# Optimization experiments

Hardware: AMD Instinct MI355X
Metric: run time of the kernel (lower is better)

The kernel has to match this reference:

```python
import jax, jax.numpy as jnp
import numpy as np

NUM_USERS = 100000
USER_EMB_DIM = 64
PROC_DIM = 128          # Dense(128) embedding_processor
NUM_SHARDS = 16
MEM_SIZE = 512          # memory slots per shard
WORD_SIZE = 64
NUM_READS = 4
INPUT_SIZE = 256
B, S = 256, 128
IN_DIM = INPUT_SIZE + PROC_DIM  # combined controller input width


def setup_inputs() -> dict:
    key = jax.random.key(0)
    k = jax.random.split(key, 7)
    x = jax.random.normal(k[0], (B, S, INPUT_SIZE), dtype=jnp.float32)
    user_id = jax.random.randint(k[1], (B,), 0, NUM_USERS, dtype=jnp.int64)
    user_emb_table = jax.random.normal(k[2], (NUM_USERS, USER_EMB_DIM), dtype=jnp.float32) * 0.02
    W_proc = jax.random.normal(k[3], (USER_EMB_DIM, PROC_DIM), dtype=jnp.float32) * (1.0 / np.sqrt(USER_EMB_DIM))
    b_proc = jnp.zeros((PROC_DIM,), dtype=jnp.float32)
    # per-shard parameters: query projection + memory matrix (the shard's state)
    Wq = jax.random.normal(k[4], (NUM_SHARDS, IN_DIM, NUM_READS * WORD_SIZE), dtype=jnp.float32) * (1.0 / np.sqrt(IN_DIM))
    memory = jax.random.normal(k[5], (NUM_SHARDS, MEM_SIZE, WORD_SIZE), dtype=jnp.float32)
    return {"x": x, "user_id": user_id, "user_emb_table": user_emb_table,
            "W_proc": W_proc, "b_proc": b_proc, "Wq": Wq, "memory": memory}


def reference(x, user_id, user_emb_table, W_proc, b_proc, Wq, memory):
    # user embedding lookup + Dense processor
    ue = user_emb_table[user_id]                       # [B, E]
    pe = ue @ W_proc + b_proc                          # [B, PROC_DIM]
    # broadcast the processed embedding across the sequence and concat on features
    pe_seq = jnp.broadcast_to(pe[:, None, :], (x.shape[0], x.shape[1], pe.shape[-1]))
    combined = jnp.concatenate([x, pe_seq], axis=-1)   # [B, S, IN_DIM]
    # shard routing (irregular gather of per-shard params)
    sid = user_id % NUM_SHARDS                         # [B]
    Wq_g = Wq[sid]                                     # [B, IN_DIM, R*W]
    mem_g = memory[sid]                                # [B, M, W]
    # per-sample shard forward: content-based read
    q = jnp.einsum('bsi,bio->bso', combined, Wq_g)     # [B, S, R*W]
    q = q.reshape(q.shape[0], q.shape[1], NUM_READS, WORD_SIZE)
    scores = jnp.einsum('bsrw,bmw->bsrm', q, mem_g)    # [B, S, R, M]
    wts = jax.nn.softmax(scores, axis=-1)
    read_words = jnp.einsum('bsrm,bmw->bsrw', wts, mem_g)  # [B, S, R, W]
    # original code keeps final_states[-1] (last sample's state)
    final_state = wts[-1]                              # [S, R, M]
    return read_words, final_state
```

## Files before the change

### kernel.cpp

```cpp
#include <hip/hip_runtime.h>
#include <math.h>

#define BB 256
#define SSEQ 128
#define INPUT 256
#define PD 128
#define EE 64
#define RW 256
#define MM 512
#define WW 64
#define KD 384

typedef _Float16 half8 __attribute__((ext_vector_type(8)));
typedef __fp16 fp16x2 __attribute__((ext_vector_type(2)));
typedef float float4v __attribute__((ext_vector_type(4)));

#define LOG2E 1.44269504088896f
#define OUT1 8388608u

#define MEMT_OFF 65536
#define F32_OFF  131072
#define LDS_BYTES (131072 + 3840)
#define UE_O 0
#define PE_O 64
#define QPE_O 192
#define QP_O 448

union H8 { half8 h8; unsigned int u[4]; uint4 u4; };

__device__ __forceinline__ unsigned int pk2(float a, float b) {
    union { fp16x2 h; unsigned int u; } p;
    p.h = __builtin_amdgcn_cvt_pkrtz(a, b);
    return p.u;
}

__global__ void wqt_kernel(const float* __restrict__ Wq, _Float16* __restrict__ WqT) {
    __shared__ float tile[64][65];
    const int kt = blockIdx.x, nt = blockIdx.y, sid = blockIdx.z;
    const float* src = Wq + (size_t)sid*KD*RW + (size_t)(kt*64)*RW + nt*64;
    for (int i = 0; i < 16; ++i) {
        int idx = i*256 + threadIdx.x;
        int kk = idx >> 6, nn = idx & 63;
        tile[kk][nn] = src[(size_t)kk*RW + nn];
    }
    __syncthreads();
    _Float16* dst = WqT + (size_t)sid*RW*KD + (size_t)(nt*64)*KD + kt*64;
    for (int i = 0; i < 16; ++i) {
        int idx = i*256 + threadIdx.x;
        int nn = idx >> 6, kk = idx & 63;
        dst[(size_t)nn*KD + kk] = (_Float16)tile[kk][nn];
    }
}

__global__ void __launch_bounds__(512, 2)
attn_kernel(const float* __restrict__ x, const int* __restrict__ user_id,
            const float* __restrict__ uet, const float* __restrict__ W_proc,
            const float* __restrict__ b_proc, const float* __restrict__ Wq,
            const float* __restrict__ memG, const _Float16* __restrict__ WqT,
            int useWqT, float* __restrict__ out)
{
    extern __shared__ char smraw[];
    unsigned short* smemu = (unsigned short*)smraw;
    uint4* sm128 = (uint4*)smraw;
    float* smf = (float*)(smraw + F32_OFF);

    const int t = threadIdx.x;
    const int b = blockIdx.x;
    const int halfb = blockIdx.y;
    const int lane = t & 63, wv = t >> 6;
    const int n16 = lane & 15, quad = lane >> 4;
    const int r = wv & 3, sq = wv >> 2;
    const int s0 = halfb*64 + sq*32;
    const int swz = n16 & 7;

    const int uid = user_id[b];
    const int sid = uid & 15;
    const float* memB = memG + (size_t)sid * (MM*WW);

    if (t < EE) smf[UE_O + t] = uet[(size_t)uid*EE + t];

    for (int i = 0; i < 8; ++i) {
        int id = t + i*512;
        int m = id >> 3, cw = id & 7;
        const float* g = memB + m*64 + cw*8;
        float4 a0 = *(const float4*)g;
        float4 a1 = *(const float4*)(g + 4);
        int c2 = cw ^ (m & 7);
        sm128[(m*128 + (c2<<4)) >> 4] =
            make_uint4(pk2(a0.x,a0.y), pk2(a0.z,a0.w), pk2(a1.x,a1.y), pk2(a1.z,a1.w));
    }
    __syncthreads();

    for (int i = 0; i < 8; ++i) {
        int id = t + i*512;
        int w = id & 63, cm = id >> 6;
        unsigned int uu[4];
        #pragma unroll
        for (int p = 0; p < 4; ++p) {
            int m0 = cm*8 + 2*p, m1 = m0 + 1;
            unsigned short lo = smemu[m0*64 + (((w>>3) ^ (m0&7))<<3) + (w&7)];
            unsigned short hi = smemu[m1*64 + (((w>>3) ^ (m1&7))<<3) + (w&7)];
            uu[p] = (unsigned int)lo | ((unsigned int)hi << 16);
        }
        sm128[(MEMT_OFF + w*1024 + ((cm ^ (w&7))<<4)) >> 4] = make_uint4(uu[0],uu[1],uu[2],uu[3]);
    }
    if (t < PD) {
        float a = b_proc[t];
        #pragma unroll
        for (int e = 0; e < EE; ++e) a = fmaf(smf[UE_O + e], W_proc[e*PD + t], a);
        smf[PE_O + t] = a;
    }
    __syncthreads();
    {
        int n = t & 255, h = t >> 8;
        float s = 0.f;
        const float* wr = Wq + (size_t)sid*KD*RW + (size_t)(256 + h*64)*RW + n;
        #pragma unroll 8
        for (int k = 0; k < 64; ++k) s = fmaf(smf[PE_O + h*64 + k], wr[(size_t)k*RW], s);
        smf[QP_O + h*256 + n] = s;
    }
    __syncthreads();
    if (t < 256) smf[QPE_O + t] = LOG2E * (smf[QP_O + t] + smf[QP_O + 256 + t]);
    __syncthreads();


    float4v qacc[4][2];
    #pragma unroll
    for (int mt = 0; mt < 4; ++mt)
        #pragma unroll
        for (int nt = 0; nt < 2; ++nt) qacc[mt][nt] = (float4v)0.f;

    const float* xB = x + (size_t)(b*SSEQ + s0) * INPUT;
    for (int kc = 0; kc < 8; ++kc) {
        H8 afr[4];
        if (useWqT) {
            const _Float16* wt0 = WqT + (size_t)sid*RW*KD + (size_t)(r*64)*KD + kc*32 + quad*8;
            #pragma unroll
            for (int mt = 0; mt < 4; ++mt)
                afr[mt].u4 = *(const uint4*)(wt0 + (size_t)(mt*16 + n16)*KD);
        } else {
            const float* wq0 = Wq + (size_t)sid*KD*RW + (size_t)(kc*32 + quad*8)*RW + r*64 + n16;
            #pragma unroll
            for (int mt = 0; mt < 4; ++mt)
                #pragma unroll
                for (int p = 0; p < 4; ++p)
                    afr[mt].u[p] = pk2(wq0[(size_t)(2*p)*RW + mt*16],
                                       wq0[(size_t)(2*p+1)*RW + mt*16]);
        }
        H8 bfr[2];
        #pragma unroll
        for (int nt = 0; nt < 2; ++nt) {
            const float* xg = xB + (size_t)(nt*16 + n16)*INPUT + kc*32 + quad*8;
            float4 a0 = *(const float4*)xg;
            float4 a1 = *(const float4*)(xg + 4);
            bfr[nt].u[0] = pk2(a0.x*LOG2E, a0.y*LOG2E);
            bfr[nt].u[1] = pk2(a0.z*LOG2E, a0.w*LOG2E);
            bfr[nt].u[2] = pk2(a1.x*LOG2E, a1.y*LOG2E);
            bfr[nt].u[3] = pk2(a1.z*LOG2E, a1.w*LOG2E);
        }
        #pragma unroll
        for (int mt = 0; mt < 4; ++mt)
            #pragma unroll
            for (int nt = 0; nt < 2; ++nt)
                qacc[mt][nt] = __builtin_amdgcn_mfma_f32_16x16x32_f16(afr[mt].h8, bfr[nt].h8, qacc[mt][nt], 0, 0, 0);
    }
    #pragma unroll
    for (int mt = 0; mt < 4; ++mt)
        #pragma unroll
        for (int reg = 0; reg < 4; ++reg) {
            float qv = smf[QPE_O + r*64 + mt*16 + quad*4 + reg];
            #pragma unroll
            for (int nt = 0; nt < 2; ++nt) qacc[mt][nt][reg] += qv;
        }
    unsigned int pkq[4][2][2];
    #pragma unroll
    for (int mt = 0; mt < 4; ++mt)
        #pragma unroll
        for (int nt = 0; nt < 2; ++nt) {
            pkq[mt][nt][0] = pk2(qacc[mt][nt][0], qacc[mt][nt][1]);
            pkq[mt][nt][1] = pk2(qacc[mt][nt][2], qacc[mt][nt][3]);
        }
    unsigned int bq[2][2][4];
    #pragma unroll
    for (int kc2 = 0; kc2 < 2; ++kc2)
        #pragma unroll
        for (int nt = 0; nt < 2; ++nt)
            #pragma unroll
            for (int p = 0; p < 4; ++p) {
                int qp = ((quad & 1) << 1) | (p >> 1);
                int src = n16 + (qp << 4);
                int sr = p & 1;
                int lo  = __shfl((int)pkq[kc2*2    ][nt][sr], src, 64);
                int hiv = __shfl((int)pkq[kc2*2 + 1][nt][sr], src, 64);
                bq[kc2][nt][p] = (unsigned int)((quad < 2) ? lo : hiv);
            }

    float4v Oa[4][2];
    #pragma unroll
    for (int wt = 0; wt < 4; ++wt)
        #pragma unroll
        for (int nt = 0; nt < 2; ++nt) Oa[wt][nt] = (float4v)0.f;
    float Ml[2] = {-1e30f, -1e30f}, ll[2] = {0.f, 0.f};

    for (int mtile = 0; mtile < 16; ++mtile) {
        float4v Sa[2][2];
        #pragma unroll
        for (int msub = 0; msub < 2; ++msub)
            #pragma unroll
            for (int nt = 0; nt < 2; ++nt) Sa[msub][nt] = (float4v)0.f;
        #pragma unroll
        for (int msub = 0; msub < 2; ++msub) {
            int m = mtile*32 + msub*16 + n16;
            #pragma unroll
            for (int kc2 = 0; kc2 < 2; ++kc2) {
                H8 af; af.u4 = sm128[(m*128 + (((kc2*4 + quad) ^ swz) << 4)) >> 4];
                #pragma unroll
                for (int nt = 0; nt < 2; ++nt) {
                    H8 bf; bf.u[0]=bq[kc2][nt][0]; bf.u[1]=bq[kc2][nt][1];
                           bf.u[2]=bq[kc2][nt][2]; bf.u[3]=bq[kc2][nt][3];
                    Sa[msub][nt] = __builtin_amdgcn_mfma_f32_16x16x32_f16(af.h8, bf.h8, Sa[msub][nt], 0, 0, 0);
                }
            }
        }
        unsigned int pkP[2][2][2];
        #pragma unroll
        for (int nt = 0; nt < 2; ++nt) {
            float tm = Sa[0][nt][0];
            #pragma unroll
            for (int g = 1; g < 4; ++g) tm = fmaxf(tm, Sa[0][nt][g]);
            #pragma unroll
            for (int g = 0; g < 4; ++g) tm = fmaxf(tm, Sa[1][nt][g]);
            tm = fmaxf(tm, __shfl_xor(tm, 16, 64));
            tm = fmaxf(tm, __shfl_xor(tm, 32, 64));
            float Mn = fmaxf(Ml[nt], tm);
            float al = __builtin_amdgcn_exp2f(Ml[nt] - Mn);
            float pv[2][4]; float ts = 0.f;
            #pragma unroll
            for (int msub = 0; msub < 2; ++msub)
                #pragma unroll
                for (int g = 0; g < 4; ++g) {
                    pv[msub][g] = __builtin_amdgcn_exp2f(Sa[msub][nt][g] - Mn);
                    ts += pv[msub][g];
                }
            ts += __shfl_xor(ts, 16, 64);
            ts += __shfl_xor(ts, 32, 64);
            ll[nt] = al*ll[nt] + ts;
            Ml[nt] = Mn;
            pkP[0][nt][0] = pk2(pv[0][0], pv[0][1]); pkP[0][nt][1] = pk2(pv[0][2], pv[0][3]);
            pkP[1][nt][0] = pk2(pv[1][0], pv[1][1]); pkP[1][nt][1] = pk2(pv[1][2], pv[1][3]);
            #pragma unroll
            for (int wt = 0; wt < 4; ++wt)
                #pragma unroll
                for (int g = 0; g < 4; ++g) Oa[wt][nt][g] *= al;
        }
        unsigned int bp[2][4];
        #pragma unroll
        for (int nt = 0; nt < 2; ++nt)
            #pragma unroll
            for (int p = 0; p < 4; ++p) {
                int qp = ((quad & 1) << 1) | (p >> 1);
                int src = n16 + (qp << 4);
                int sr = p & 1;
                int lo  = __shfl((int)pkP[0][nt][sr], src, 64);
                int hiv = __shfl((int)pkP[1][nt][sr], src, 64);
                bp[nt][p] = (unsigned int)((quad < 2) ? lo : hiv);
            }
        #pragma unroll
        for (int wt = 0; wt < 4; ++wt) {
            H8 af; af.u4 = sm128[(MEMT_OFF + (wt*16 + n16)*1024 + (((mtile*4 + quad) ^ swz) << 4)) >> 4];
            #pragma unroll
            for (int nt = 0; nt < 2; ++nt) {
                H8 bf; bf.u[0]=bp[nt][0]; bf.u[1]=bp[nt][1]; bf.u[2]=bp[nt][2]; bf.u[3]=bp[nt][3];
                Oa[wt][nt] = __builtin_amdgcn_mfma_f32_16x16x32_f16(af.h8, bf.h8, Oa[wt][nt], 0, 0, 0);
            }
        }
    }

    #pragma unroll
    for (int nt = 0; nt < 2; ++nt) {
        float inv = 1.0f / ll[nt];
        int s = s0 + nt*16 + n16;
        #pragma unroll
        for (int wt = 0; wt < 4; ++wt) {
            float4 o = make_float4(Oa[wt][nt][0]*inv, Oa[wt][nt][1]*inv,
                                   Oa[wt][nt][2]*inv, Oa[wt][nt][3]*inv);
            *(float4*)&out[((size_t)(b*SSEQ + s)*4 + r)*WW + wt*16 + quad*4] = o;
        }
    }

    if (b == BB - 1) {
        for (int mtile = 0; mtile < 16; ++mtile) {
            float4v Sa[2][2];
            #pragma unroll
            for (int msub = 0; msub < 2; ++msub)
                #pragma unroll
                for (int nt = 0; nt < 2; ++nt) Sa[msub][nt] = (float4v)0.f;
            #pragma unroll
            for (int msub = 0; msub < 2; ++msub) {
                int m = mtile*32 + msub*16 + n16;
                #pragma unroll
                for (int kc2 = 0; kc2 < 2; ++kc2) {
                    H8 af; af.u4 = sm128[(m*128 + (((kc2*4 + quad) ^ swz) << 4)) >> 4];
                    #pragma unroll
                    for (int nt = 0; nt < 2; ++nt) {
                        H8 bf; bf.u[0]=bq[kc2][nt][0]; bf.u[1]=bq[kc2][nt][1];
                               bf.u[2]=bq[kc2][nt][2]; bf.u[3]=bq[kc2][nt][3];
                        Sa[msub][nt] = __builtin_amdgcn_mfma_f32_16x16x32_f16(af.h8, bf.h8, Sa[msub][nt], 0, 0, 0);
                    }
                }
            }
            #pragma unroll
            for (int nt = 0; nt < 2; ++nt) {
                float inv = 1.0f / ll[nt];
                int s = s0 + nt*16 + n16;
                size_t base = (size_t)OUT1 + ((size_t)(s*4 + r) << 9);
                #pragma unroll
                for (int msub = 0; msub < 2; ++msub) {
                    float4 w4 = make_float4(
                        __builtin_amdgcn_exp2f(Sa[msub][nt][0] - Ml[nt]) * inv,
                        __builtin_amdgcn_exp2f(Sa[msub][nt][1] - Ml[nt]) * inv,
                        __builtin_amdgcn_exp2f(Sa[msub][nt][2] - Ml[nt]) * inv,
                        __builtin_amdgcn_exp2f(Sa[msub][nt][3] - Ml[nt]) * inv);
                    *(float4*)&out[base + mtile*32 + msub*16 + quad*4] = w4;
                }
            }
        }
    }
}

extern "C" void kernel_launch(void* const* d_in, const int* in_sizes, int n_in,
                              void* d_out, int out_size, void* d_ws, size_t ws_size,
                              hipStream_t stream) {
    const float* x    = (const float*)d_in[0];
    const int*   uid  = (const int*)  d_in[1];
    const float* uet  = (const float*)d_in[2];
    const float* Wp   = (const float*)d_in[3];
    const float* bp   = (const float*)d_in[4];
    const float* Wq   = (const float*)d_in[5];
    const float* mem  = (const float*)d_in[6];
    float* out = (float*)d_out;

    const size_t need = (size_t)16 * RW * KD * 2;
    int useWqT = (ws_size >= need) ? 1 : 0;
    _Float16* WqT = (_Float16*)d_ws;

    if (useWqT) {
        dim3 g0(KD/64, RW/64, 16);
        wqt_kernel<<<g0, 256, 0, stream>>>(Wq, WqT);
    }

    (void)hipFuncSetAttribute((const void*)attn_kernel,
                              hipFuncAttributeMaxDynamicSharedMemorySize, LDS_BYTES);
    dim3 grid(BB, 2);
    attn_kernel<<<grid, 512, LDS_BYTES, stream>>>(x, uid, uet, Wp, bp, Wq, mem, WqT, useWqT, out);
}
```

Measured before the change: 198.0 us.

## Precompute per-shard fp16 memory images and use one 1024-thread block per sample

A prep kernel now converts each shard's memory to fp16 once, in both swizzled row-major and transposed layouts, stores them in workspace, and also builds the transposed fp16 Wq. The attention kernel copies the ready image into LDS instead of converting and transposing per block. It also merges the two sequence halves into one 1024-thread block, so the memory load is no longer repeated for the two halves of each sample. The risk is lower occupancy, since each 1024-thread block needs about 134KB of LDS, and an extra workspace round trip for the images.

```diff
diff --git a/kernel.cpp b/kernel.cpp
--- a/kernel.cpp
+++ b/kernel.cpp
@@ -20,11 +20,16 @@
 
 #define MEMT_OFF 65536
 #define F32_OFF  131072
-#define LDS_BYTES (131072 + 3840)
+#define LDS_BYTES (131072 + 6144)
 #define UE_O 0
 #define PE_O 64
 #define QPE_O 192
 #define QP_O 448
+
+#define IMG_SHARD 131072
+#define WQT_OFF  (16*IMG_SHARD)
+#define WQT_BYTES ((size_t)16*RW*KD*2)
+#define PREP_LDS 65536
 
 union H8 { half8 h8; unsigned int u[4]; uint4 u4; };
 
@@ -34,30 +39,70 @@
     return p.u;
 }
 
-__global__ void wqt_kernel(const float* __restrict__ Wq, _Float16* __restrict__ WqT) {
-    __shared__ float tile[64][65];
-    const int kt = blockIdx.x, nt = blockIdx.y, sid = blockIdx.z;
-    const float* src = Wq + (size_t)sid*KD*RW + (size_t)(kt*64)*RW + nt*64;
-    for (int i = 0; i < 16; ++i) {
-        int idx = i*256 + threadIdx.x;
-        int kk = idx >> 6, nn = idx & 63;
-        tile[kk][nn] = src[(size_t)kk*RW + nn];
-    }
-    __syncthreads();
-    _Float16* dst = WqT + (size_t)sid*RW*KD + (size_t)(nt*64)*KD + kt*64;
-    for (int i = 0; i < 16; ++i) {
-        int idx = i*256 + threadIdx.x;
-        int nn = idx >> 6, kk = idx & 63;
-        dst[(size_t)nn*KD + kk] = (_Float16)tile[kk][nn];
+__global__ void prep_kernel(const float* __restrict__ Wq, const float* __restrict__ memG,
+                            char* __restrict__ ws, int useImg, int useWqT) {
+    extern __shared__ char sm[];
+    const int blk = blockIdx.x;
+    const int t = threadIdx.x;
+    if (blk < 384) {
+        if (!useWqT) return;
+        float (*tile)[65] = (float (*)[65])sm;
+        const int kt = blk % 6, ntb = (blk / 6) & 3, sid = blk / 24;
+        const float* src = Wq + (size_t)sid*KD*RW + (size_t)(kt*64)*RW + ntb*64;
+        for (int i = 0; i < 16; ++i) {
+            int idx = i*256 + t;
+            int kk = idx >> 6, nn = idx & 63;
+            tile[kk][nn] = src[(size_t)kk*RW + nn];
+        }
+        __syncthreads();
+        _Float16* dst = (_Float16*)(ws + WQT_OFF) + (size_t)sid*RW*KD + (size_t)(ntb*64)*KD + kt*64;
+        for (int i = 0; i < 16; ++i) {
+            int idx = i*256 + t;
+            int nn = idx >> 6, kk = idx & 63;
+            dst[(size_t)nn*KD + kk] = (_Float16)tile[kk][nn];
+        }
+    } else {
+        if (!useImg) return;
+        const int sid = blk - 384;
+        const float* memB = memG + (size_t)sid * (MM*WW);
+        uint4* lds128 = (uint4*)sm;
+        unsigned short* ldsu = (unsigned short*)sm;
+        uint4* wsA = (uint4*)(ws + (size_t)sid*IMG_SHARD);
+        uint4* wsB = wsA + 4096;
+        for (int i = 0; i < 16; ++i) {
+            int id = i*256 + t;
+            int m = id >> 3, cw = id & 7;
+            const float* g = memB + m*64 + cw*8;
+            float4 a0 = *(const float4*)g;
+            float4 a1 = *(const float4*)(g + 4);
+            uint4 v = make_uint4(pk2(a0.x,a0.y), pk2(a0.z,a0.w), pk2(a1.x,a1.y), pk2(a1.z,a1.w));
+            int chunk = m*8 + (cw ^ (m & 7));
+            lds128[chunk] = v;
+            wsA[chunk] = v;
+        }
+        __syncthreads();
+        for (int i = 0; i < 16; ++i) {
+            int id = i*256 + t;
+            int w = id & 63, cm = id >> 6;
+            unsigned int uu[4];
+            #pragma unroll
+            for (int p = 0; p < 4; ++p) {
+                int m0 = cm*8 + 2*p, m1 = m0 + 1;
+                unsigned short lo = ldsu[m0*64 + (((w>>3) ^ (m0&7))<<3) + (w&7)];
+                unsigned short hi = ldsu[m1*64 + (((w>>3) ^ (m1&7))<<3) + (w&7)];
+                uu[p] = (unsigned int)lo | ((unsigned int)hi << 16);
+            }
+            wsB[w*64 + (cm ^ (w & 7))] = make_uint4(uu[0], uu[1], uu[2], uu[3]);
+        }
     }
 }
 
-__global__ void __launch_bounds__(512, 2)
+__global__ void __launch_bounds__(1024, 4)
 attn_kernel(const float* __restrict__ x, const int* __restrict__ user_id,
             const float* __restrict__ uet, const float* __restrict__ W_proc,
             const float* __restrict__ b_proc, const float* __restrict__ Wq,
-            const float* __restrict__ memG, const _Float16* __restrict__ WqT,
-            int useWqT, float* __restrict__ out)
+            const float* __restrict__ memG, const char* __restrict__ ws,
+            int useImg, int useWqT, float* __restrict__ out)
 {
     extern __shared__ char smraw[];
     unsigned short* smemu = (unsigned short*)smraw;
@@ -66,11 +111,10 @@
 
     const int t = threadIdx.x;
     const int b = blockIdx.x;
-    const int halfb = blockIdx.y;
     const int lane = t & 63, wv = t >> 6;
     const int n16 = lane & 15, quad = lane >> 4;
     const int r = wv & 3, sq = wv >> 2;
-    const int s0 = halfb*64 + sq*32;
+    const int s0 = sq * 32;
     const int swz = n16 & 7;
 
     const int uid = user_id[b];
@@ -79,31 +123,39 @@
 
     if (t < EE) smf[UE_O + t] = uet[(size_t)uid*EE + t];
 
-    for (int i = 0; i < 8; ++i) {
-        int id = t + i*512;
-        int m = id >> 3, cw = id & 7;
-        const float* g = memB + m*64 + cw*8;
-        float4 a0 = *(const float4*)g;
-        float4 a1 = *(const float4*)(g + 4);
-        int c2 = cw ^ (m & 7);
-        sm128[(m*128 + (c2<<4)) >> 4] =
-            make_uint4(pk2(a0.x,a0.y), pk2(a0.z,a0.w), pk2(a1.x,a1.y), pk2(a1.z,a1.w));
+    if (useImg) {
+        const uint4* img = (const uint4*)(ws + (size_t)sid*IMG_SHARD);
+        #pragma unroll
+        for (int i = 0; i < 8; ++i) {
+            int id = i*1024 + t;
+            sm128[id] = img[id];
+        }
+    } else {
+        for (int i = 0; i < 4; ++i) {
+            int id = t + i*1024;
+            int m = id >> 3, cw = id & 7;
+            const float* g = memB + m*64 + cw*8;
+            float4 a0 = *(const float4*)g;
+            float4 a1 = *(const float4*)(g + 4);
+            sm128[m*8 + (cw ^ (m & 7))] =
+                make_uint4(pk2(a0.x,a0.y), pk2(a0.z,a0.w), pk2(a1.x,a1.y), pk2(a1.z,a1.w));
+        }
+        __syncthreads();
+        for (int i = 0; i < 4; ++i) {
+            int id = t + i*1024;
+            int w = id & 63, cm = id >> 6;
+            unsigned int uu[4];
+            #pragma unroll
+            for (int p = 0; p < 4; ++p) {
+                int m0 = cm*8 + 2*p, m1 = m0 + 1;
+                unsigned short lo = smemu[m0*64 + (((w>>3) ^ (m0&7))<<3) + (w&7)];
+                unsigned short hi = smemu[m1*64 + (((w>>3) ^ (m1&7))<<3) + (w&7)];
+                uu[p] = (unsigned int)lo | ((unsigned int)hi << 16);
+            }
+            sm128[(MEMT_OFF >> 4) + w*64 + (cm ^ (w & 7))] = make_uint4(uu[0],uu[1],uu[2],uu[3]);
+        }
     }
     __syncthreads();
-
-    for (int i = 0; i < 8; ++i) {
-        int id = t + i*512;
-        int w = id & 63, cm = id >> 6;
-        unsigned int uu[4];
-        #pragma unroll
-        for (int p = 0; p < 4; ++p) {
-            int m0 = cm*8 + 2*p, m1 = m0 + 1;
-            unsigned short lo = smemu[m0*64 + (((w>>3) ^ (m0&7))<<3) + (w&7)];
-            unsigned short hi = smemu[m1*64 + (((w>>3) ^ (m1&7))<<3) + (w&7)];
-            uu[p] = (unsigned int)lo | ((unsigned int)hi << 16);
-        }
-        sm128[(MEMT_OFF + w*1024 + ((cm ^ (w&7))<<4)) >> 4] = make_uint4(uu[0],uu[1],uu[2],uu[3]);
-    }
     if (t < PD) {
         float a = b_proc[t];
         #pragma unroll
@@ -114,13 +166,14 @@
     {
         int n = t & 255, h = t >> 8;
         float s = 0.f;
-        const float* wr = Wq + (size_t)sid*KD*RW + (size_t)(256 + h*64)*RW + n;
+        const float* wr = Wq + (size_t)sid*KD*RW + (size_t)(256 + h*32)*RW + n;
         #pragma unroll 8
-        for (int k = 0; k < 64; ++k) s = fmaf(smf[PE_O + h*64 + k], wr[(size_t)k*RW], s);
+        for (int k = 0; k < 32; ++k) s = fmaf(smf[PE_O + h*32 + k], wr[(size_t)k*RW], s);
         smf[QP_O + h*256 + n] = s;
     }
     __syncthreads();
-    if (t < 256) smf[QPE_O + t] = LOG2E * (smf[QP_O + t] + smf[QP_O + 256 + t]);
+    if (t < 256) smf[QPE_O + t] = LOG2E * (smf[QP_O + t] + smf[QP_O + 256 + t]
+                                         + smf[QP_O + 512 + t] + smf[QP_O + 768 + t]);
     __syncthreads();
 
 
@@ -134,7 +187,8 @@
     for (int kc = 0; kc < 8; ++kc) {
         H8 afr[4];
         if (useWqT) {
-            const _Float16* wt0 = WqT + (size_t)sid*RW*KD + (size_t)(r*64)*KD + kc*32 + quad*8;
+            const _Float16* wt0 = (const _Float16*)(ws + WQT_OFF)
+                                + (size_t)sid*RW*KD + (size_t)(r*64)*KD + kc*32 + quad*8;
             #pragma unroll
             for (int mt = 0; mt < 4; ++mt)
                 afr[mt].u4 = *(const uint4*)(wt0 + (size_t)(mt*16 + n16)*KD);
@@ -213,7 +267,7 @@
             int m = mtile*32 + msub*16 + n16;
             #pragma unroll
             for (int kc2 = 0; kc2 < 2; ++kc2) {
-                H8 af; af.u4 = sm128[(m*128 + (((kc2*4 + quad) ^ swz) << 4)) >> 4];
+                H8 af; af.u4 = sm128[m*8 + ((kc2*4 + quad) ^ swz)];
                 #pragma unroll
                 for (int nt = 0; nt < 2; ++nt) {
                     H8 bf; bf.u[0]=bq[kc2][nt][0]; bf.u[1]=bq[kc2][nt][1];
@@ -267,7 +321,7 @@
             }
         #pragma unroll
         for (int wt = 0; wt < 4; ++wt) {
-            H8 af; af.u4 = sm128[(MEMT_OFF + (wt*16 + n16)*1024 + (((mtile*4 + quad) ^ swz) << 4)) >> 4];
+            H8 af; af.u4 = sm128[(MEMT_OFF >> 4) + (wt*16 + n16)*64 + ((mtile*4 + quad) ^ swz)];
             #pragma unroll
             for (int nt = 0; nt < 2; ++nt) {
                 H8 bf; bf.u[0]=bp[nt][0]; bf.u[1]=bp[nt][1]; bf.u[2]=bp[nt][2]; bf.u[3]=bp[nt][3];
@@ -300,7 +354,7 @@
                 int m = mtile*32 + msub*16 + n16;
                 #pragma unroll
                 for (int kc2 = 0; kc2 < 2; ++kc2) {
-                    H8 af; af.u4 = sm128[(m*128 + (((kc2*4 + quad) ^ swz) << 4)) >> 4];
+                    H8 af; af.u4 = sm128[m*8 + ((kc2*4 + quad) ^ swz)];
                     #pragma unroll
                     for (int nt = 0; nt < 2; ++nt) {
                         H8 bf; bf.u[0]=bq[kc2][nt][0]; bf.u[1]=bq[kc2][nt][1];
@@ -339,18 +393,19 @@
     const float* Wq   = (const float*)d_in[5];
     const float* mem  = (const float*)d_in[6];
     float* out = (float*)d_out;
-
-    const size_t need = (size_t)16 * RW * KD * 2;
-    int useWqT = (ws_size >= need) ? 1 : 0;
-    _Float16* WqT = (_Float16*)d_ws;
-
-    if (useWqT) {
-        dim3 g0(KD/64, RW/64, 16);
-        wqt_kernel<<<g0, 256, 0, stream>>>(Wq, WqT);
-    }
-
+    char* ws = (char*)d_ws;
+
+    int useImg = (ws_size >= (size_t)WQT_OFF) ? 1 : 0;
+    int useWqT = (ws_size >= (size_t)WQT_OFF + WQT_BYTES) ? 1 : 0;
+
+    (void)hipFuncSetAttribute((const void*)prep_kernel,
+                              hipFuncAttributeMaxDynamicSharedMemorySize, PREP_LDS);
     (void)hipFuncSetAttribute((const void*)attn_kernel,
                               hipFuncAttributeMaxDynamicSharedMemorySize, LDS_BYTES);
-    dim3 grid(BB, 2);
-    attn_kernel<<<grid, 512, LDS_BYTES, stream>>>(x, uid, uet, Wp, bp, Wq, mem, WqT, useWqT, out);
+
+    if (useImg || useWqT)
+        prep_kernel<<<400, 256, PREP_LDS, stream>>>(Wq, mem, ws, useImg, useWqT);
+
+    attn_kernel<<<BB, 1024, LDS_BYTES, stream>>>(x, uid, uet, Wp, bp, Wq, mem, ws,
+                                                 useImg, useWqT, out);
 }
```

Result: faster. 175.2 us (-11.5%).

## Merge sequence halves into one 1024-thread block and stage Wq in LDS

Applied to the files above, without the earlier changes.

The separate Wq transpose/convert kernel is dropped. Each block now has 1024 threads and covers the full 128-step sequence for one sample, so memory and Wq are loaded once per sample rather than once per half. The x-part of Wq (256x256) is converted to fp16 and staged into LDS in MFMA-fragment layout. After the query projection, the same LDS region is reused for the memory matrix and its transpose. The trade-offs are extra barriers, a serialized Wq-then-memory staging phase, a launch bound of 1024 threads with 4 blocks requested, and only 256 blocks in the grid.

```diff
diff --git a/kernel.cpp b/kernel.cpp
--- a/kernel.cpp
+++ b/kernel.cpp
@@ -20,7 +20,7 @@
 
 #define MEMT_OFF 65536
 #define F32_OFF  131072
-#define LDS_BYTES (131072 + 3840)
+#define LDS_BYTES (131072 + 6144)
 #define UE_O 0
 #define PE_O 64
 #define QPE_O 192
@@ -34,76 +34,42 @@
     return p.u;
 }
 
-__global__ void wqt_kernel(const float* __restrict__ Wq, _Float16* __restrict__ WqT) {
-    __shared__ float tile[64][65];
-    const int kt = blockIdx.x, nt = blockIdx.y, sid = blockIdx.z;
-    const float* src = Wq + (size_t)sid*KD*RW + (size_t)(kt*64)*RW + nt*64;
-    for (int i = 0; i < 16; ++i) {
-        int idx = i*256 + threadIdx.x;
-        int kk = idx >> 6, nn = idx & 63;
-        tile[kk][nn] = src[(size_t)kk*RW + nn];
-    }
-    __syncthreads();
-    _Float16* dst = WqT + (size_t)sid*RW*KD + (size_t)(nt*64)*KD + kt*64;
-    for (int i = 0; i < 16; ++i) {
-        int idx = i*256 + threadIdx.x;
-        int nn = idx >> 6, kk = idx & 63;
-        dst[(size_t)nn*KD + kk] = (_Float16)tile[kk][nn];
-    }
-}
-
-__global__ void __launch_bounds__(512, 2)
+__global__ void __launch_bounds__(1024, 4)
 attn_kernel(const float* __restrict__ x, const int* __restrict__ user_id,
             const float* __restrict__ uet, const float* __restrict__ W_proc,
             const float* __restrict__ b_proc, const float* __restrict__ Wq,
-            const float* __restrict__ memG, const _Float16* __restrict__ WqT,
-            int useWqT, float* __restrict__ out)
+            const float* __restrict__ memG, float* __restrict__ out)
 {
     extern __shared__ char smraw[];
     unsigned short* smemu = (unsigned short*)smraw;
-    uint4* sm128 = (uint4*)smraw;
-    float* smf = (float*)(smraw + F32_OFF);
+    unsigned int*   smw   = (unsigned int*)smraw;
+    uint4*          sm128 = (uint4*)smraw;
+    float*          smf   = (float*)(smraw + F32_OFF);
 
     const int t = threadIdx.x;
     const int b = blockIdx.x;
-    const int halfb = blockIdx.y;
     const int lane = t & 63, wv = t >> 6;
     const int n16 = lane & 15, quad = lane >> 4;
     const int r = wv & 3, sq = wv >> 2;
-    const int s0 = halfb*64 + sq*32;
+    const int s0 = sq * 32;
     const int swz = n16 & 7;
 
     const int uid = user_id[b];
     const int sid = uid & 15;
     const float* memB = memG + (size_t)sid * (MM*WW);
+    const float* wqX  = Wq + (size_t)sid * KD * RW;
 
     if (t < EE) smf[UE_O + t] = uet[(size_t)uid*EE + t];
 
-    for (int i = 0; i < 8; ++i) {
-        int id = t + i*512;
-        int m = id >> 3, cw = id & 7;
-        const float* g = memB + m*64 + cw*8;
-        float4 a0 = *(const float4*)g;
-        float4 a1 = *(const float4*)(g + 4);
-        int c2 = cw ^ (m & 7);
-        sm128[(m*128 + (c2<<4)) >> 4] =
-            make_uint4(pk2(a0.x,a0.y), pk2(a0.z,a0.w), pk2(a1.x,a1.y), pk2(a1.z,a1.w));
-    }
-    __syncthreads();
-
-    for (int i = 0; i < 8; ++i) {
-        int id = t + i*512;
-        int w = id & 63, cm = id >> 6;
-        unsigned int uu[4];
-        #pragma unroll
-        for (int p = 0; p < 4; ++p) {
-            int m0 = cm*8 + 2*p, m1 = m0 + 1;
-            unsigned short lo = smemu[m0*64 + (((w>>3) ^ (m0&7))<<3) + (w&7)];
-            unsigned short hi = smemu[m1*64 + (((w>>3) ^ (m1&7))<<3) + (w&7)];
-            uu[p] = (unsigned int)lo | ((unsigned int)hi << 16);
-        }
-        sm128[(MEMT_OFF + w*1024 + ((cm ^ (w&7))<<4)) >> 4] = make_uint4(uu[0],uu[1],uu[2],uu[3]);
-    }
+    for (int i = 0; i < 32; ++i) {
+        int idx = i*1024 + t;
+        int n = idx & 255, kp = idx >> 8;
+        float w0 = wqX[(size_t)(2*kp)    *RW + n];
+        float w1 = wqX[(size_t)(2*kp + 1)*RW + n];
+        smw[((((kp>>2)*256 + n) << 2) | (kp & 3))] = pk2(w0, w1);
+    }
+    __syncthreads();
+
     if (t < PD) {
         float a = b_proc[t];
         #pragma unroll
@@ -114,15 +80,15 @@
     {
         int n = t & 255, h = t >> 8;
         float s = 0.f;
-        const float* wr = Wq + (size_t)sid*KD*RW + (size_t)(256 + h*64)*RW + n;
+        const float* wr = wqX + (size_t)(256 + h*32)*RW + n;
         #pragma unroll 8
-        for (int k = 0; k < 64; ++k) s = fmaf(smf[PE_O + h*64 + k], wr[(size_t)k*RW], s);
+        for (int k = 0; k < 32; ++k) s = fmaf(smf[PE_O + h*32 + k], wr[(size_t)k*RW], s);
         smf[QP_O + h*256 + n] = s;
     }
     __syncthreads();
-    if (t < 256) smf[QPE_O + t] = LOG2E * (smf[QP_O + t] + smf[QP_O + 256 + t]);
-    __syncthreads();
-
+    if (t < 256) smf[QPE_O + t] = LOG2E * (smf[QP_O + t] + smf[QP_O + 256 + t]
+                                         + smf[QP_O + 512 + t] + smf[QP_O + 768 + t]);
+    __syncthreads();
 
     float4v qacc[4][2];
     #pragma unroll
@@ -133,20 +99,9 @@
     const float* xB = x + (size_t)(b*SSEQ + s0) * INPUT;
     for (int kc = 0; kc < 8; ++kc) {
         H8 afr[4];
-        if (useWqT) {
-            const _Float16* wt0 = WqT + (size_t)sid*RW*KD + (size_t)(r*64)*KD + kc*32 + quad*8;
-            #pragma unroll
-            for (int mt = 0; mt < 4; ++mt)
-                afr[mt].u4 = *(const uint4*)(wt0 + (size_t)(mt*16 + n16)*KD);
-        } else {
-            const float* wq0 = Wq + (size_t)sid*KD*RW + (size_t)(kc*32 + quad*8)*RW + r*64 + n16;
-            #pragma unroll
-            for (int mt = 0; mt < 4; ++mt)
-                #pragma unroll
-                for (int p = 0; p < 4; ++p)
-                    afr[mt].u[p] = pk2(wq0[(size_t)(2*p)*RW + mt*16],
-                                       wq0[(size_t)(2*p+1)*RW + mt*16]);
-        }
+        #pragma unroll
+        for (int mt = 0; mt < 4; ++mt)
+            afr[mt].u4 = sm128[(kc*4 + quad)*256 + r*64 + mt*16 + n16];
         H8 bfr[2];
         #pragma unroll
         for (int nt = 0; nt < 2; ++nt) {
@@ -194,6 +149,32 @@
                 int hiv = __shfl((int)pkq[kc2*2 + 1][nt][sr], src, 64);
                 bq[kc2][nt][p] = (unsigned int)((quad < 2) ? lo : hiv);
             }
+    __syncthreads();
+
+    for (int i = 0; i < 4; ++i) {
+        int id = t + i*1024;
+        int m = id >> 3, cw = id & 7;
+        const float* g = memB + m*64 + cw*8;
+        float4 a0 = *(const float4*)g;
+        float4 a1 = *(const float4*)(g + 4);
+        sm128[m*8 + (cw ^ (m & 7))] =
+            make_uint4(pk2(a0.x,a0.y), pk2(a0.z,a0.w), pk2(a1.x,a1.y), pk2(a1.z,a1.w));
+    }
+    __syncthreads();
+    for (int i = 0; i < 4; ++i) {
+        int id = t + i*1024;
+        int w = id & 63, cm = id >> 6;
+        unsigned int uu[4];
+        #pragma unroll
+        for (int p = 0; p < 4; ++p) {
+            int m0 = cm*8 + 2*p, m1 = m0 + 1;
+            unsigned short lo = smemu[m0*64 + (((w>>3) ^ (m0&7))<<3) + (w&7)];
+            unsigned short hi = smemu[m1*64 + (((w>>3) ^ (m1&7))<<3) + (w&7)];
+            uu[p] = (unsigned int)lo | ((unsigned int)hi << 16);
+        }
+        sm128[(MEMT_OFF >> 4) + w*64 + (cm ^ (w & 7))] = make_uint4(uu[0],uu[1],uu[2],uu[3]);
+    }
+    __syncthreads();
 
     float4v Oa[4][2];
     #pragma unroll
@@ -213,7 +194,7 @@
             int m = mtile*32 + msub*16 + n16;
             #pragma unroll
             for (int kc2 = 0; kc2 < 2; ++kc2) {
-                H8 af; af.u4 = sm128[(m*128 + (((kc2*4 + quad) ^ swz) << 4)) >> 4];
+                H8 af; af.u4 = sm128[m*8 + ((kc2*4 + quad) ^ swz)];
                 #pragma unroll
                 for (int nt = 0; nt < 2; ++nt) {
                     H8 bf; bf.u[0]=bq[kc2][nt][0]; bf.u[1]=bq[kc2][nt][1];
@@ -267,7 +248,7 @@
             }
         #pragma unroll
         for (int wt = 0; wt < 4; ++wt) {
-            H8 af; af.u4 = sm128[(MEMT_OFF + (wt*16 + n16)*1024 + (((mtile*4 + quad) ^ swz) << 4)) >> 4];
+            H8 af; af.u4 = sm128[(MEMT_OFF >> 4) + (wt*16 + n16)*64 + ((mtile*4 + quad) ^ swz)];
             #pragma unroll
             for (int nt = 0; nt < 2; ++nt) {
                 H8 bf; bf.u[0]=bp[nt][0]; bf.u[1]=bp[nt][1]; bf.u[2]=bp[nt][2]; bf.u[3]=bp[nt][3];
@@ -300,7 +281,7 @@
                 int m = mtile*32 + msub*16 + n16;
                 #pragma unroll
                 for (int kc2 = 0; kc2 < 2; ++kc2) {
-                    H8 af; af.u4 = sm128[(m*128 + (((kc2*4 + quad) ^ swz) << 4)) >> 4];
+                    H8 af; af.u4 = sm128[m*8 + ((kc2*4 + quad) ^ swz)];
                     #pragma unroll
                     for (int nt = 0; nt < 2; ++nt) {
                         H8 bf; bf.u[0]=bq[kc2][nt][0]; bf.u[1]=bq[kc2][nt][1];
@@ -340,17 +321,7 @@
     const float* mem  = (const float*)d_in[6];
     float* out = (float*)d_out;
 
-    const size_t need = (size_t)16 * RW * KD * 2;
-    int useWqT = (ws_size >= need) ? 1 : 0;
-    _Float16* WqT = (_Float16*)d_ws;
-
-    if (useWqT) {
-        dim3 g0(KD/64, RW/64, 16);
-        wqt_kernel<<<g0, 256, 0, stream>>>(Wq, WqT);
-    }
-
     (void)hipFuncSetAttribute((const void*)attn_kernel,
                               hipFuncAttributeMaxDynamicSharedMemorySize, LDS_BYTES);
-    dim3 grid(BB, 2);
-    attn_kernel<<<grid, 512, LDS_BYTES, stream>>>(x, uid, uet, Wp, bp, Wq, mem, WqT, useWqT, out);
+    attn_kernel<<<BB, 1024, LDS_BYTES, stream>>>(x, uid, uet, Wp, bp, Wq, mem, out);
 }
```

After: 168.7 us. 1.17x faster.
